# Optimization experiments

Hardware: AMD Instinct MI355X
Metric: run time of the kernel (lower is better)

The kernel has to match this reference:

```python
import jax, jax.numpy as jnp
import numpy as np

D_MODEL = 1024
ED = 2048        # d_inner = expand_factor * d_model
N = 16           # d_state
DT_RANK = 64     # ceil(d_model/16)
K = 4            # d_conv
B_SZ = 4
L = 512


def _causal_depthwise_conv(u, w, b):
    # u: [B, L, ED], w: [ED, 1, K], b: [ED]
    xc = jnp.transpose(u, (0, 2, 1))  # [B, ED, L]
    xc = jax.lax.conv_general_dilated(
        xc, w, window_strides=(1,), padding=[(K - 1, 0)],
        feature_group_count=ED, dimension_numbers=('NCH', 'OIH', 'NCH'))
    xc = xc + b[None, :, None]
    return jnp.transpose(xc, (0, 2, 1))  # [B, L, ED]


def _ssm_branch(xz_half, z, conv_w, conv_b, Wx, Wdt, b_dt, A_log, Dp):
    # xz_half, z: [B, L, ED]
    x = jax.nn.silu(_causal_depthwise_conv(xz_half, conv_w, conv_b))
    dbc = x @ Wx.T  # [B, L, dt_rank + 2N]
    delta = dbc[..., :DT_RANK]
    Bm = dbc[..., DT_RANK:DT_RANK + N]
    Cm = dbc[..., DT_RANK + N:]
    delta = jax.nn.softplus(delta @ Wdt.T + b_dt)  # [B, L, ED]
    A = -jnp.exp(A_log)  # [ED, N]
    dA = jnp.exp(delta[..., None] * A)                        # [B, L, ED, N]
    bx = (delta[..., None] * Bm[:, :, None, :]) * x[..., None]  # [B, L, ED, N]
    dA_t = jnp.transpose(dA, (1, 0, 2, 3))
    bx_t = jnp.transpose(bx, (1, 0, 2, 3))
    c_t = jnp.transpose(Cm, (1, 0, 2))  # [L, B, N]
    h0 = jnp.zeros((x.shape[0], ED, N), dtype=x.dtype)

    def step(h, inp):
        dAi, bxi, ci = inp
        h = dAi * h + bxi
        return h, jnp.einsum('ben,bn->be', h, ci)

    _, ys = jax.lax.scan(step, h0, (dA_t, bx_t, c_t))
    y = jnp.transpose(ys, (1, 0, 2)) + Dp * x  # D skip connection
    return y * jax.nn.silu(z)                  # gate


def _mamba_block(x, W_in, conv_w, conv_b, Wx, Wdt, b_dt, A_log, Dp,
                 conv_w_b, conv_b_b, Wx_b, Wdt_b, b_dt_b, A_log_b, Dp_b, W_out):
    xz = x @ W_in.T  # [B, L, 2*ED]
    xf, zf = xz[..., :ED], xz[..., ED:]
    y = _ssm_branch(xf, zf, conv_w, conv_b, Wx, Wdt, b_dt, A_log, Dp)
    xz_r = xz[:, ::-1, :]
    xb, zb = xz_r[..., :ED], xz_r[..., ED:]
    y_b = _ssm_branch(xb, zb, conv_w_b, conv_b_b, Wx_b, Wdt_b, b_dt_b, A_log_b, Dp_b)
    y = (y + y_b[:, ::-1, :]) * 0.5
    return y @ W_out.T


def setup_inputs() -> dict:
    key = jax.random.key(0)
    ks = jax.random.split(key, 20)
    s = lambda k, shp, sc: jax.random.normal(k, shp, dtype=jnp.float32) * sc
    dt = jnp.exp(jax.random.uniform(ks[15], (ED,)) * (np.log(0.1) - np.log(0.001)) + np.log(0.001))
    dt = jnp.clip(dt, 1e-4, None)
    inv_dt = dt + jnp.log(-jnp.expm1(-dt))
    A_init = jnp.log(jnp.tile(jnp.arange(1, N + 1, dtype=jnp.float32), (ED, 1)))
    return {
        'x': s(ks[0], (B_SZ, L, D_MODEL), 1.0),
        'W_in': s(ks[1], (2 * ED, D_MODEL), D_MODEL ** -0.5),
        'conv_w': s(ks[2], (ED, 1, K), K ** -0.5),
        'conv_b': s(ks[3], (ED,), 0.02),
        'Wx': s(ks[4], (DT_RANK + 2 * N, ED), ED ** -0.5),
        'Wdt': jax.random.uniform(ks[5], (ED, DT_RANK), minval=-DT_RANK ** -0.5, maxval=DT_RANK ** -0.5),
        'b_dt': inv_dt,
        'A_log': A_init,
        'Dp': jnp.ones((ED,), dtype=jnp.float32),
        'conv_w_b': s(ks[6], (ED, 1, K), K ** -0.5),
        'conv_b_b': s(ks[7], (ED,), 0.02),
        'Wx_b': s(ks[8], (DT_RANK + 2 * N, ED), ED ** -0.5),
        'Wdt_b': jax.random.uniform(ks[9], (ED, DT_RANK), minval=-DT_RANK ** -0.5, maxval=DT_RANK ** -0.5),
        'b_dt_b': inv_dt,
        'A_log_b': A_init,
        'Dp_b': jnp.ones((ED,), dtype=jnp.float32),
        'W_out': s(ks[10], (D_MODEL, ED), ED ** -0.5),
    }


def reference(x, W_in, conv_w, conv_b, Wx, Wdt, b_dt, A_log, Dp,
              conv_w_b, conv_b_b, Wx_b, Wdt_b, b_dt_b, A_log_b, Dp_b, W_out):
    return _mamba_block(x, W_in, conv_w, conv_b, Wx, Wdt, b_dt, A_log, Dp,
                        conv_w_b, conv_b_b, Wx_b, Wdt_b, b_dt_b, A_log_b, Dp_b, W_out)
```

## Files before the change

### kernel.cpp

```cpp
#include <hip/hip_runtime.h>
#include <hip/hip_bf16.h>
#include <stdint.h>

typedef unsigned short ushort_t;
typedef __attribute__((ext_vector_type(8))) short short8;
typedef __attribute__((ext_vector_type(4))) float f32x4;

__device__ __forceinline__ float b2f(ushort_t u) {
    union { uint32_t i; float f; } v; v.i = ((uint32_t)u) << 16; return v.f;
}
__device__ __forceinline__ ushort_t f2b(float f) {
    union { float f; uint32_t i; } v; v.f = f;
    uint32_t r = v.i + 0x7fff + ((v.i >> 16) & 1);
    return (ushort_t)(r >> 16);
}

#if __has_builtin(__builtin_amdgcn_exp2f)
#define EXP2(x) __builtin_amdgcn_exp2f(x)
#else
#define EXP2(x) __expf((x) * 0.69314718056f)
#endif

__device__ __forceinline__ void ll16(const ushort_t* g, ushort_t* l) {
    __builtin_amdgcn_global_load_lds(
        (const __attribute__((address_space(1))) uint32_t*)g,
        (__attribute__((address_space(3))) uint32_t*)l, 16, 0, 0);
}

template <int CTRL>
__device__ __forceinline__ float dpp_add(float p) {
    int v = __builtin_amdgcn_update_dpp(0, __float_as_int(p), CTRL, 0xF, 0xF, true);
    return p + __int_as_float(v);
}
#define DPP_XOR1 0xB1
#define DPP_XOR2 0x4E
#define DPP_HMIR 0x141

__device__ __forceinline__ void epi_wave_f32(
    float* sw, const f32x4* accg, float* dst0, int ldc, int lane)
{
    const int quad = lane >> 4, lr = lane & 15;
#pragma unroll
    for (int j = 0; j < 4; j++)
#pragma unroll
        for (int r = 0; r < 4; r++)
            sw[(quad * 4 + r) * 64 + j * 16 + lr] = accg[j][r];
    __asm__ volatile("s_waitcnt lgkmcnt(0)" ::: "memory");
#pragma unroll
    for (int t = 0; t < 4; t++) {
        int row = t * 4 + quad;
        float4 v = *(const float4*)(&sw[row * 64 + lr * 4]);
        *(float4*)(dst0 + (size_t)row * ldc + lr * 4) = v;
    }
}

__device__ __forceinline__ void epi_wave_b16(
    float* sw, const f32x4* accg, ushort_t* dst0, int ldc, int lane)
{
    const int quad = lane >> 4, lr = lane & 15;
#pragma unroll
    for (int j = 0; j < 4; j++)
#pragma unroll
        for (int r = 0; r < 4; r++)
            sw[(quad * 4 + r) * 64 + j * 16 + lr] = accg[j][r];
    __asm__ volatile("s_waitcnt lgkmcnt(0)" ::: "memory");
#pragma unroll
    for (int t = 0; t < 4; t++) {
        int row = t * 4 + quad;
        float4 v = *(const float4*)(&sw[row * 64 + lr * 4]);
        ushort4 o; o.x = f2b(v.x); o.y = f2b(v.y); o.z = f2b(v.z); o.w = f2b(v.w);
        *(ushort4*)(dst0 + (size_t)row * ldc + lr * 4) = o;
    }
}

struct CastSeg { const float4* src; ushort4* dst; };
struct CastArgs { CastSeg seg[7]; int start[8]; };

__global__ __launch_bounds__(256) void cast_multi(CastArgs a)
{
    int g = blockIdx.x * 256 + threadIdx.x;
    if (g >= a.start[7]) return;
    int s = 0;
#pragma unroll
    for (int i = 1; i < 7; i++) s += (g >= a.start[i]);
    int i = g - a.start[s];
    float4 v = a.seg[s].src[i];
    ushort4 o;
    o.x = f2b(v.x); o.y = f2b(v.y); o.z = f2b(v.z); o.w = f2b(v.w);
    a.seg[s].dst[i] = o;
}

#define BK 32

__global__ __launch_bounds__(256) void gemm_g1(
    const ushort_t* __restrict__ A, int lda,
    const ushort_t* __restrict__ B, int ldb,
    ushort_t* __restrict__ Cout, int ldc, int Kd)
{
    __shared__ ushort_t As[128 * BK];
    __shared__ ushort_t Bs[128 * BK];
    __shared__ float sepi[4][1024];

    const int tid  = threadIdx.x;
    const int m0   = blockIdx.y * 128;
    const int n0   = blockIdx.x * 128;
    const int wv   = tid >> 6;
    const int lane = tid & 63;
    const int wm   = (wv >> 1) * 64;
    const int wn   = (wv & 1) * 64;
    const int lr   = lane & 15;
    const int quad = lane >> 4;

    f32x4 acc[4][4];
#pragma unroll
    for (int i = 0; i < 4; i++)
#pragma unroll
        for (int j = 0; j < 4; j++) acc[i][j] = f32x4{0.f, 0.f, 0.f, 0.f};

    const int srA = wv * 32 + (lane >> 2);
    const int scA = (lane & 3) * 8;

    for (int k0 = 0; k0 < Kd; k0 += BK) {
        ll16(A + (size_t)(m0 + srA) * lda + k0 + scA,      &As[wv * 1024]);
        ll16(A + (size_t)(m0 + srA + 16) * lda + k0 + scA, &As[wv * 1024 + 512]);
        ll16(B + (size_t)(n0 + srA) * ldb + k0 + scA,      &Bs[wv * 1024]);
        ll16(B + (size_t)(n0 + srA + 16) * ldb + k0 + scA, &Bs[wv * 1024 + 512]);
        __syncthreads();

        short8 af[4], bf[4];
#pragma unroll
        for (int i = 0; i < 4; i++)
            af[i] = *(const short8*)(&As[(wm + i * 16 + lr) * BK + quad * 8]);
#pragma unroll
        for (int j = 0; j < 4; j++)
            bf[j] = *(const short8*)(&Bs[(wn + j * 16 + lr) * BK + quad * 8]);
#pragma unroll
        for (int i = 0; i < 4; i++)
#pragma unroll
            for (int j = 0; j < 4; j++)
                acc[i][j] = __builtin_amdgcn_mfma_f32_16x16x32_bf16(af[i], bf[j], acc[i][j], 0, 0, 0);
        __syncthreads();
    }

#pragma unroll
    for (int g = 0; g < 4; g++)
        epi_wave_b16(sepi[wv], acc[g],
                     Cout + (size_t)(m0 + wm + g * 16) * ldc + n0 + wn, ldc, lane);
}

__global__ __launch_bounds__(256) void gemm_g4(
    const ushort_t* __restrict__ A, int lda,
    const ushort_t* __restrict__ B, int ldb,
    float* __restrict__ Cout, int ldc, int Kd)
{
    __shared__ ushort_t As[64 * BK];
    __shared__ ushort_t Bs[128 * BK];
    __shared__ float sepi[4][1024];

    const int tid  = threadIdx.x;
    const int m0   = blockIdx.y * 64;
    const int n0   = blockIdx.x * 128;
    const int wv   = tid >> 6;
    const int lane = tid & 63;
    const int wm   = (wv >> 1) * 32;
    const int wn   = (wv & 1) * 64;
    const int lr   = lane & 15;
    const int quad = lane >> 4;

    f32x4 acc[2][4];
#pragma unroll
    for (int i = 0; i < 2; i++)
#pragma unroll
        for (int j = 0; j < 4; j++) acc[i][j] = f32x4{0.f, 0.f, 0.f, 0.f};

    const int srA = wv * 16 + (lane >> 2);
    const int srB = wv * 32 + (lane >> 2);
    const int sc  = (lane & 3) * 8;

    for (int k0 = 0; k0 < Kd; k0 += BK) {
        ll16(A + (size_t)(m0 + srA) * lda + k0 + sc,      &As[wv * 512]);
        ll16(B + (size_t)(n0 + srB) * ldb + k0 + sc,      &Bs[wv * 1024]);
        ll16(B + (size_t)(n0 + srB + 16) * ldb + k0 + sc, &Bs[wv * 1024 + 512]);
        __syncthreads();

        short8 af[2], bf[4];
#pragma unroll
        for (int i = 0; i < 2; i++)
            af[i] = *(const short8*)(&As[(wm + i * 16 + lr) * BK + quad * 8]);
#pragma unroll
        for (int j = 0; j < 4; j++)
            bf[j] = *(const short8*)(&Bs[(wn + j * 16 + lr) * BK + quad * 8]);
#pragma unroll
        for (int i = 0; i < 2; i++)
#pragma unroll
            for (int j = 0; j < 4; j++)
                acc[i][j] = __builtin_amdgcn_mfma_f32_16x16x32_bf16(af[i], bf[j], acc[i][j], 0, 0, 0);
        __syncthreads();
    }

#pragma unroll
    for (int g = 0; g < 2; g++)
        epi_wave_f32(sepi[wv], acc[g],
                     Cout + (size_t)(m0 + wm + g * 16) * ldc + n0 + wn, ldc, lane);
}

__global__ __launch_bounds__(256) void gemm_g2(
    const ushort_t* __restrict__ xc, const ushort_t* __restrict__ wx,
    float* __restrict__ part)
{
    __shared__ ushort_t As[128 * BK];
    __shared__ ushort_t Bs[128 * BK];
    __shared__ float sepi[4][1024];

    const int sk = blockIdx.x, mb = blockIdx.y, br = blockIdx.z;
    const ushort_t* A = xc + (size_t)br * 2048 * 2048;
    const ushort_t* B = wx + (size_t)br * 96 * 2048;
    float* C = part + (size_t)(sk * 2 + br) * 2048 * 96;
    const int m0 = mb * 128;
    const int kb = sk * 256;

    const int tid  = threadIdx.x;
    const int wv   = tid >> 6;
    const int lane = tid & 63;
    const int wm   = (wv >> 1) * 64;
    const int wn   = (wv & 1) * 64;
    const int lr   = lane & 15;
    const int quad = lane >> 4;

    f32x4 acc[4][4];
#pragma unroll
    for (int i = 0; i < 4; i++)
#pragma unroll
        for (int j = 0; j < 4; j++) acc[i][j] = f32x4{0.f, 0.f, 0.f, 0.f};

    const int srA = wv * 32 + (lane >> 2);
    const int sc  = (lane & 3) * 8;

    for (int k0 = kb; k0 < kb + 256; k0 += BK) {
        ll16(A + (size_t)(m0 + srA) * 2048 + k0 + sc,      &As[wv * 1024]);
        ll16(A + (size_t)(m0 + srA + 16) * 2048 + k0 + sc, &As[wv * 1024 + 512]);
        ll16(B + (size_t)(srA) * 2048 + k0 + sc,           &Bs[wv * 1024]);
        ll16(B + (size_t)(srA + 16) * 2048 + k0 + sc,      &Bs[wv * 1024 + 512]);
        __syncthreads();

        short8 af[4], bf[4];
#pragma unroll
        for (int i = 0; i < 4; i++)
            af[i] = *(const short8*)(&As[(wm + i * 16 + lr) * BK + quad * 8]);
#pragma unroll
        for (int j = 0; j < 4; j++)
            bf[j] = *(const short8*)(&Bs[(wn + j * 16 + lr) * BK + quad * 8]);
#pragma unroll
        for (int i = 0; i < 4; i++)
#pragma unroll
            for (int j = 0; j < 4; j++)
                acc[i][j] = __builtin_amdgcn_mfma_f32_16x16x32_bf16(af[i], bf[j], acc[i][j], 0, 0, 0);
        __syncthreads();
    }

    float* sw = sepi[wv];
#pragma unroll
    for (int g = 0; g < 4; g++) {
#pragma unroll
        for (int j = 0; j < 4; j++)
#pragma unroll
            for (int r = 0; r < 4; r++)
                sw[(quad * 4 + r) * 64 + j * 16 + lr] = acc[g][j][r];
        __asm__ volatile("s_waitcnt lgkmcnt(0)" ::: "memory");
        int col = wn + lr * 4;
#pragma unroll
        for (int t = 0; t < 4; t++) {
            int row = t * 4 + quad;
            if (col < 96) {
                float4 v = *(const float4*)(&sw[row * 64 + lr * 4]);
                *(float4*)(C + (size_t)(m0 + wm + g * 16 + row) * 96 + col) = v;
            }
        }
    }
}

__global__ __launch_bounds__(256) void reduce_dbc(
    const float4* __restrict__ part, ushort4* __restrict__ dbc16)
{
    int g = blockIdx.x * 256 + threadIdx.x;
    const int S = 2 * 2048 * 96 / 4;
    float4 r = part[g];
#pragma unroll
    for (int i = 1; i < 8; i++) {
        float4 p = part[g + i * S];
        r.x += p.x; r.y += p.y; r.z += p.z; r.w += p.w;
    }
    ushort4 o; o.x = f2b(r.x); o.y = f2b(r.y); o.z = f2b(r.z); o.w = f2b(r.w);
    dbc16[g] = o;
}

__global__ __launch_bounds__(256) void gemm_g3(
    const ushort_t* __restrict__ dbc16, const ushort_t* __restrict__ wdt,
    ushort_t* __restrict__ delta,
    const float* __restrict__ bdt_f, const float* __restrict__ bdt_b)
{
    __shared__ ushort_t As[128 * BK];
    __shared__ ushort_t Bs[128 * BK];
    __shared__ float sepi[4][1024];

    const int br = blockIdx.z;
    const ushort_t* A = dbc16 + (size_t)br * 2048 * 96;
    const ushort_t* B = wdt + (size_t)br * 2048 * 64;
    ushort_t* C = delta + (size_t)br * 2048 * 2048;
    const float* bias = br ? bdt_b : bdt_f;

    const int tid  = threadIdx.x;
    const int m0   = blockIdx.y * 128;
    const int n0   = blockIdx.x * 128;
    const int wv   = tid >> 6;
    const int lane = tid & 63;
    const int wm   = (wv >> 1) * 64;
    const int wn   = (wv & 1) * 64;
    const int lr   = lane & 15;
    const int quad = lane >> 4;

    f32x4 acc[4][4];
#pragma unroll
    for (int i = 0; i < 4; i++)
#pragma unroll
        for (int j = 0; j < 4; j++) acc[i][j] = f32x4{0.f, 0.f, 0.f, 0.f};

    const int srA = wv * 32 + (lane >> 2);
    const int sc  = (lane & 3) * 8;

    for (int k0 = 0; k0 < 64; k0 += BK) {
        ll16(A + (size_t)(m0 + srA) * 96 + k0 + sc,       &As[wv * 1024]);
        ll16(A + (size_t)(m0 + srA + 16) * 96 + k0 + sc,  &As[wv * 1024 + 512]);
        ll16(B + (size_t)(n0 + srA) * 64 + k0 + sc,       &Bs[wv * 1024]);
        ll16(B + (size_t)(n0 + srA + 16) * 64 + k0 + sc,  &Bs[wv * 1024 + 512]);
        __syncthreads();

        short8 af[4], bf[4];
#pragma unroll
        for (int i = 0; i < 4; i++)
            af[i] = *(const short8*)(&As[(wm + i * 16 + lr) * BK + quad * 8]);
#pragma unroll
        for (int j = 0; j < 4; j++)
            bf[j] = *(const short8*)(&Bs[(wn + j * 16 + lr) * BK + quad * 8]);
#pragma unroll
        for (int i = 0; i < 4; i++)
#pragma unroll
            for (int j = 0; j < 4; j++)
                acc[i][j] = __builtin_amdgcn_mfma_f32_16x16x32_bf16(af[i], bf[j], acc[i][j], 0, 0, 0);
        __syncthreads();
    }

    float bn[4];
#pragma unroll
    for (int j = 0; j < 4; j++) bn[j] = bias[n0 + wn + j * 16 + lr];
#pragma unroll
    for (int g = 0; g < 4; g++)
#pragma unroll
        for (int j = 0; j < 4; j++)
#pragma unroll
            for (int r = 0; r < 4; r++) {
                float x = acc[g][j][r] + bn[j];
                float sp = fmaxf(x, 0.f) + __logf(1.f + __expf(-fabsf(x)));
                acc[g][j][r] = sp;
            }

#pragma unroll
    for (int g = 0; g < 4; g++)
        epi_wave_b16(sepi[wv], acc[g],
                     C + (size_t)(m0 + wm + g * 16) * 2048 + n0 + wn, 2048, lane);
}

__global__ __launch_bounds__(256) void conv_silu_kernel(
    const ushort_t* __restrict__ xz,
    const float* __restrict__ w_f, const float* __restrict__ cb_f,
    const float* __restrict__ w_b, const float* __restrict__ cb_b,
    ushort_t* __restrict__ xc16)
{
    int g = blockIdx.x * 256 + threadIdx.x;
    int e  = g & 2047;
    int t  = (g >> 11) & 511;
    int b  = (g >> 20) & 3;
    int br = g >> 22;

    const float* w  = br ? w_b  : w_f;
    const float* cb = br ? cb_b : cb_f;

    float acc = cb[e];
    float4 wv = *(const float4*)(w + e * 4);
    float wk[4] = { wv.x, wv.y, wv.z, wv.w };

#pragma unroll
    for (int k = 0; k < 4; k++) {
        int tp = t - 3 + k;
        if (tp >= 0) {
            int row = br ? (511 - tp) : tp;
            acc += wk[k] * b2f(xz[((size_t)(b * 512 + row)) * 4096 + e]);
        }
    }
    float s = acc / (1.f + __expf(-acc));
    xc16[g] = f2b(s);
}

__global__ __launch_bounds__(256) void scan_kernel(
    const ushort_t* __restrict__ delta,
    const ushort_t* __restrict__ xc,
    const ushort_t* __restrict__ dbc16,
    const ushort_t* __restrict__ xz,
    const float* __restrict__ Alog_f, const float* __restrict__ Alog_b,
    const float* __restrict__ Dp_f,   const float* __restrict__ Dp_b,
    ushort_t* __restrict__ yf, ushort_t* __restrict__ yb)
{
    const int blk = blockIdx.x;
    const int eg = blk & 63;
    const int b  = (blk >> 6) & 3;
    const int br = blk >> 8;
    const int e0 = eg * 32;

    const int tid = threadIdx.x;
    const int n2  = tid & 7;
    const int el  = tid >> 3;
    const int e   = e0 + el;

    const float* Alog = br ? Alog_b : Alog_f;
    const float* Dpp  = br ? Dp_b   : Dp_f;
    const float A0 = -__expf(Alog[e * 16 + n2]) * 1.44269504f;
    const float A1 = -__expf(Alog[e * 16 + n2 + 8]) * 1.44269504f;

    size_t tb = ((size_t)br * 4 + b) * 512;
    const ushort_t* dlt  = delta + tb * 2048;
    const ushort_t* xcb  = xc    + tb * 2048;
    const ushort_t* dbcb = dbc16 + tb * 96;
    ushort_t* y = (br ? yb : yf) + (size_t)b * 512 * 2048;

    __shared__ float    sd [2][32][68];
    __shared__ float    sdx[2][32][68];
    __shared__ float    sB [2][16][68];
    __shared__ float    sC [2][16][68];
    __shared__ float    sy [2][64][36];

    const int stt = tid >> 2;
    const int seg = tid & 3;
    const int swz = seg * 8;
    const int scol = stt ^ swz;

    float4 rD0 = *(const float4*)(Dpp + e0 + seg * 8);
    float4 rD1 = *(const float4*)(Dpp + e0 + seg * 8 + 4);

    uint4 rdx, rx, rbc, rz;
    uint4 rx_c, rx_f, rz_c, rz_f;

    auto load_regs = [&](int c) {
        int t0 = c * 64;
        rdx = *(const uint4*)(dlt + (size_t)(t0 + stt) * 2048 + e0 + seg * 8);
        rx  = *(const uint4*)(xcb + (size_t)(t0 + stt) * 2048 + e0 + seg * 8);
        rbc = *(const uint4*)(dbcb + (size_t)(t0 + stt) * 96 + 64 + seg * 8);
        int orow = br ? (511 - (t0 + stt)) : (t0 + stt);
        rz  = *(const uint4*)(xz + ((size_t)(b * 512 + orow)) * 4096 + 2048 + e0 + seg * 8);
    };
    auto write_lds = [&](int buf) {
        const uint32_t dw[4] = { rdx.x, rdx.y, rdx.z, rdx.w };
        const uint32_t xw[4] = { rx.x, rx.y, rx.z, rx.w };
#pragma unroll
        for (int k = 0; k < 4; k++) {
            float d0 = b2f((ushort_t)(dw[k] & 0xffff));
            float d1 = b2f((ushort_t)(dw[k] >> 16));
            float x0 = b2f((ushort_t)(xw[k] & 0xffff));
            float x1 = b2f((ushort_t)(xw[k] >> 16));
            sd [buf][seg * 8 + 2 * k][scol]     = d0;
            sd [buf][seg * 8 + 2 * k + 1][scol] = d1;
            sdx[buf][seg * 8 + 2 * k][scol]     = d0 * x0;
            sdx[buf][seg * 8 + 2 * k + 1][scol] = d1 * x1;
        }
        float* arr = (seg < 2) ? &sB[buf][0][0] : &sC[buf][0][0];
        const int rbase = (seg & 1) * 8;
        const uint32_t bw[4] = { rbc.x, rbc.y, rbc.z, rbc.w };
#pragma unroll
        for (int k = 0; k < 4; k++) {
            arr[(rbase + 2 * k) * 68 + scol]     = b2f((ushort_t)(bw[k] & 0xffff));
            arr[(rbase + 2 * k + 1) * 68 + scol] = b2f((ushort_t)(bw[k] >> 16));
        }
    };
    auto flush = [&](int cm1) {
        const int bufm1 = cm1 & 1;
        int row = cm1 * 64 + stt;
        const uint32_t zw[4] = { rz_f.x, rz_f.y, rz_f.z, rz_f.w };
        float zv[8];
#pragma unroll
        for (int k = 0; k < 4; k++) {
            zv[2 * k]     = b2f((ushort_t)(zw[k] & 0xffff));
            zv[2 * k + 1] = b2f((ushort_t)(zw[k] >> 16));
        }
        float4 p0 = *(const float4*)(&sy[bufm1][stt][seg * 8]);
        float4 p1 = *(const float4*)(&sy[bufm1][stt][seg * 8 + 4]);
        const float pv[8] = { p0.x, p0.y, p0.z, p0.w, p1.x, p1.y, p1.z, p1.w };
        const uint32_t xw[4] = { rx_f.x, rx_f.y, rx_f.z, rx_f.w };
        float xvv[8];
#pragma unroll
        for (int k = 0; k < 4; k++) {
            xvv[2 * k]     = b2f((ushort_t)(xw[k] & 0xffff));
            xvv[2 * k + 1] = b2f((ushort_t)(xw[k] >> 16));
        }
        const float Dv[8] = { rD0.x, rD0.y, rD0.z, rD0.w, rD1.x, rD1.y, rD1.z, rD1.w };
        uint32_t op[4];
#pragma unroll
        for (int k = 0; k < 4; k++) {
            float ga = (pv[2 * k]     + Dv[2 * k]     * xvv[2 * k])     *
                       (zv[2 * k]     / (1.f + __expf(-zv[2 * k])));
            float gb = (pv[2 * k + 1] + Dv[2 * k + 1] * xvv[2 * k + 1]) *
                       (zv[2 * k + 1] / (1.f + __expf(-zv[2 * k + 1])));
            op[k] = (uint32_t)f2b(ga) | ((uint32_t)f2b(gb) << 16);
        }
        *(uint4*)(y + (size_t)row * 2048 + e0 + seg * 8) =
            make_uint4(op[0], op[1], op[2], op[3]);
    };

    float h0 = 0.f, h1 = 0.f;
    const int sw = ((el >> 3) & 3) * 8;

    load_regs(0);
    write_lds(0);
    rx_c = rx; rz_c = rz;

    for (int c = 0; c < 8; ++c) {
        if (c < 7) load_regs(c + 1);
        __syncthreads();
        const int buf = c & 1;

        auto LDQ = [&](int tq, float4& dv, float4& dxv, float4& B0, float4& B1,
                       float4& C0, float4& C1) {
            const int tc = tq ^ sw;
            dv  = *(const float4*)(&sd [buf][el][tc]);
            dxv = *(const float4*)(&sdx[buf][el][tc]);
            B0  = *(const float4*)(&sB[buf][n2][tq]);
            B1  = *(const float4*)(&sB[buf][n2 + 8][tq ^ 8]);
            C0  = *(const float4*)(&sC[buf][n2][tq ^ 16]);
            C1  = *(const float4*)(&sC[buf][n2 + 8][tq ^ 24]);
        };

        float4 dv_p, dxv_p, B0_p, B1_p, C0_p, C1_p;
        LDQ(0, dv_p, dxv_p, B0_p, B1_p, C0_p, C1_p);

#pragma unroll 4
        for (int tq = 0; tq < 64; tq += 4) {
            const float4 dv = dv_p, dxv = dxv_p;
            const float4 B0 = B0_p, B1 = B1_p, C0 = C0_p, C1 = C1_p;
            LDQ((tq + 4) & 63, dv_p, dxv_p, B0_p, B1_p, C0_p, C1_p);

            float e00 = EXP2(dv.x * A0), e01 = EXP2(dv.y * A0);
            float e02 = EXP2(dv.z * A0), e03 = EXP2(dv.w * A0);
            float e10 = EXP2(dv.x * A1), e11 = EXP2(dv.y * A1);
            float e12 = EXP2(dv.z * A1), e13 = EXP2(dv.w * A1);

            h0 = e00 * h0 + dxv.x * B0.x;  h1 = e10 * h1 + dxv.x * B1.x;
            float p0 = h0 * C0.x + h1 * C1.x;
            h0 = e01 * h0 + dxv.y * B0.y;  h1 = e11 * h1 + dxv.y * B1.y;
            float p1 = h0 * C0.y + h1 * C1.y;
            h0 = e02 * h0 + dxv.z * B0.z;  h1 = e12 * h1 + dxv.z * B1.z;
            float p2 = h0 * C0.z + h1 * C1.z;
            h0 = e03 * h0 + dxv.w * B0.w;  h1 = e13 * h1 + dxv.w * B1.w;
            float p3 = h0 * C0.w + h1 * C1.w;

            p0 = dpp_add<DPP_XOR1>(p0); p0 = dpp_add<DPP_XOR2>(p0); p0 = dpp_add<DPP_HMIR>(p0);
            p1 = dpp_add<DPP_XOR1>(p1); p1 = dpp_add<DPP_XOR2>(p1); p1 = dpp_add<DPP_HMIR>(p1);
            p2 = dpp_add<DPP_XOR1>(p2); p2 = dpp_add<DPP_XOR2>(p2); p2 = dpp_add<DPP_HMIR>(p2);
            p3 = dpp_add<DPP_XOR1>(p3); p3 = dpp_add<DPP_XOR2>(p3); p3 = dpp_add<DPP_HMIR>(p3);

            if (n2 == 0) {
                sy[buf][tq + 0][el] = p0;
                sy[buf][tq + 1][el] = p1;
                sy[buf][tq + 2][el] = p2;
                sy[buf][tq + 3][el] = p3;
            }
        }

        if (c > 0) flush(c - 1);

        if (c < 7) {
            write_lds((c + 1) & 1);
            rx_f = rx_c; rz_f = rz_c;
            rx_c = rx;   rz_c = rz;
        } else {
            rx_f = rx_c; rz_f = rz_c;
        }
    }
    __syncthreads();
    flush(7);
}

__global__ __launch_bounds__(256) void combine_kernel(
    const uint2* __restrict__ yf, const uint2* __restrict__ yb,
    uint2* __restrict__ yc)
{
    int g = blockIdx.x * 256 + threadIdx.x;
    int e4 = g & 511;
    int t  = (g >> 9) & 511;
    int b  = g >> 18;
    uint2 a = yf[g];
    uint2 c = yb[((size_t)(b * 512 + 511 - t)) * 512 + e4];
    uint2 o;
    o.x = (uint32_t)f2b(0.5f * (b2f((ushort_t)(a.x & 0xffff)) + b2f((ushort_t)(c.x & 0xffff)))) |
          ((uint32_t)f2b(0.5f * (b2f((ushort_t)(a.x >> 16)) + b2f((ushort_t)(c.x >> 16)))) << 16);
    o.y = (uint32_t)f2b(0.5f * (b2f((ushort_t)(a.y & 0xffff)) + b2f((ushort_t)(c.y & 0xffff)))) |
          ((uint32_t)f2b(0.5f * (b2f((ushort_t)(a.y >> 16)) + b2f((ushort_t)(c.y >> 16)))) << 16);
    yc[g] = o;
}

static const size_t TT = 2048;
static const size_t OFF_XZ16  = 0;
static const size_t OFF_XC16  = OFF_XZ16  + TT*4096*2;
static const size_t OFF_DBC16 = OFF_XC16  + 2*TT*2048*2;
static const size_t OFF_DELTA = OFF_DBC16 + 2*TT*96*2;
static const size_t OFF_YF    = OFF_DELTA + 2*TT*2048*2;
static const size_t OFF_YB    = OFF_YF    + TT*2048*2;
static const size_t OFF_YC16  = OFF_YB    + TT*2048*2;
static const size_t OFF_X16   = OFF_YC16  + TT*2048*2;
static const size_t OFF_WIN16 = OFF_X16   + TT*1024*2;
static const size_t OFF_WX16  = OFF_WIN16 + 4096*1024*2;
static const size_t OFF_WDT16 = OFF_WX16  + 2*96*2048*2;
static const size_t OFF_WOUT16= OFF_WDT16 + 2*2048*64*2;
static const size_t OFF_PART  = OFF_WOUT16+ 1024*2048*2;

extern "C" void kernel_launch(void* const* d_in, const int* in_sizes, int n_in,
                              void* d_out, int out_size, void* d_ws, size_t ws_size,
                              hipStream_t stream) {
    const float* x       = (const float*)d_in[0];
    const float* W_in    = (const float*)d_in[1];
    const float* conv_w  = (const float*)d_in[2];
    const float* conv_b  = (const float*)d_in[3];
    const float* Wx      = (const float*)d_in[4];
    const float* Wdt     = (const float*)d_in[5];
    const float* b_dt    = (const float*)d_in[6];
    const float* A_log   = (const float*)d_in[7];
    const float* Dp      = (const float*)d_in[8];
    const float* conv_w_b= (const float*)d_in[9];
    const float* conv_b_b= (const float*)d_in[10];
    const float* Wx_b    = (const float*)d_in[11];
    const float* Wdt_b   = (const float*)d_in[12];
    const float* b_dt_b  = (const float*)d_in[13];
    const float* A_log_b = (const float*)d_in[14];
    const float* Dp_b    = (const float*)d_in[15];
    const float* W_out   = (const float*)d_in[16];
    float* out = (float*)d_out;

    char* ws = (char*)d_ws;
    ushort_t* xz16  = (ushort_t*)(ws + OFF_XZ16);
    ushort_t* xc16  = (ushort_t*)(ws + OFF_XC16);
    ushort_t* dbc16 = (ushort_t*)(ws + OFF_DBC16);
    ushort_t* delta = (ushort_t*)(ws + OFF_DELTA);
    ushort_t* yf    = (ushort_t*)(ws + OFF_YF);
    ushort_t* yb    = (ushort_t*)(ws + OFF_YB);
    ushort_t* yc16  = (ushort_t*)(ws + OFF_YC16);
    ushort_t* x16   = (ushort_t*)(ws + OFF_X16);
    ushort_t* win16 = (ushort_t*)(ws + OFF_WIN16);
    ushort_t* wx16  = (ushort_t*)(ws + OFF_WX16);
    ushort_t* wdt16 = (ushort_t*)(ws + OFF_WDT16);
    ushort_t* wout16= (ushort_t*)(ws + OFF_WOUT16);
    float*    part  = (float*)(ws + OFF_PART);

    dim3 blk(256);

    CastArgs ca;
    const int n4s[7] = {524288, 1048576, 49152, 49152, 32768, 32768, 524288};
    ca.seg[0] = { (const float4*)x,     (ushort4*)x16 };
    ca.seg[1] = { (const float4*)W_in,  (ushort4*)win16 };
    ca.seg[2] = { (const float4*)Wx,    (ushort4*)wx16 };
    ca.seg[3] = { (const float4*)Wx_b,  (ushort4*)(wx16 + 96 * 2048) };
    ca.seg[4] = { (const float4*)Wdt,   (ushort4*)wdt16 };
    ca.seg[5] = { (const float4*)Wdt_b, (ushort4*)(wdt16 + 2048 * 64) };
    ca.seg[6] = { (const float4*)W_out, (ushort4*)wout16 };
    ca.start[0] = 0;
    for (int i = 0; i < 7; i++) ca.start[i + 1] = ca.start[i] + n4s[i];
    cast_multi<<<(ca.start[7] + 255) / 256, blk, 0, stream>>>(ca);

    gemm_g1<<<dim3(32, 16), blk, 0, stream>>>(x16, 1024, win16, 1024, xz16, 4096, 1024);

    conv_silu_kernel<<<32768, blk, 0, stream>>>(xz16, conv_w, conv_b, conv_w_b, conv_b_b, xc16);

    gemm_g2<<<dim3(8, 16, 2), blk, 0, stream>>>(xc16, wx16, part);
    reduce_dbc<<<384, blk, 0, stream>>>((const float4*)part, (ushort4*)dbc16);

    gemm_g3<<<dim3(16, 16, 2), blk, 0, stream>>>(dbc16, wdt16, delta, b_dt, b_dt_b);

    scan_kernel<<<512, blk, 0, stream>>>(delta, xc16, dbc16, xz16, A_log, A_log_b, Dp, Dp_b, yf, yb);

    combine_kernel<<<4096, blk, 0, stream>>>((const uint2*)yf, (const uint2*)yb, (uint2*)yc16);

    gemm_g4<<<dim3(8, 32), blk, 0, stream>>>(yc16, 2048, wout16, 2048, out, 1024, 2048);
}
```

Measured before the change: 276.4 us.

## Shrink scan chunk to 32 steps, pack state as float2, raise occupancy

The selective-scan kernel now processes 32-timestep chunks instead of 64, which halves the shared-memory tiles, and requests 4 blocks per SM through launch bounds. B and C are stored interleaved in pairs so the two state halves can be updated with packed float2 arithmetic, and the swizzles are replaced by padding. The aim is higher occupancy and fewer instructions per step, which hides latency better. The cost is twice as many chunk iterations and barriers, narrower global loads, and possible register spills under the tighter bound.

Result: no change. 274.0 us (-0.9%).

```diff
diff --git a/kernel.cpp b/kernel.cpp
--- a/kernel.cpp
+++ b/kernel.cpp
@@ -5,6 +5,7 @@
 typedef unsigned short ushort_t;
 typedef __attribute__((ext_vector_type(8))) short short8;
 typedef __attribute__((ext_vector_type(4))) float f32x4;
+typedef __attribute__((ext_vector_type(2))) float f32x2;
 
 __device__ __forceinline__ float b2f(ushort_t u) {
     union { uint32_t i; float f; } v; v.i = ((uint32_t)u) << 16; return v.f;
@@ -401,7 +402,7 @@
     xc16[g] = f2b(s);
 }
 
-__global__ __launch_bounds__(256) void scan_kernel(
+__global__ __launch_bounds__(256, 4) void scan_kernel(
     const ushort_t* __restrict__ delta,
     const ushort_t* __restrict__ xc,
     const ushort_t* __restrict__ dbc16,
@@ -423,8 +424,9 @@
 
     const float* Alog = br ? Alog_b : Alog_f;
     const float* Dpp  = br ? Dp_b   : Dp_f;
-    const float A0 = -__expf(Alog[e * 16 + n2]) * 1.44269504f;
-    const float A1 = -__expf(Alog[e * 16 + n2 + 8]) * 1.44269504f;
+    f32x2 a01;
+    a01.x = -__expf(Alog[e * 16 + n2]) * 1.44269504f;
+    a01.y = -__expf(Alog[e * 16 + n2 + 8]) * 1.44269504f;
 
     size_t tb = ((size_t)br * 4 + b) * 512;
     const ushort_t* dlt  = delta + tb * 2048;
@@ -432,150 +434,146 @@
     const ushort_t* dbcb = dbc16 + tb * 96;
     ushort_t* y = (br ? yb : yf) + (size_t)b * 512 * 2048;
 
-    __shared__ float    sd [2][32][68];
-    __shared__ float    sdx[2][32][68];
-    __shared__ float    sB [2][16][68];
-    __shared__ float    sC [2][16][68];
-    __shared__ float    sy [2][64][36];
-
-    const int stt = tid >> 2;
-    const int seg = tid & 3;
-    const int swz = seg * 8;
-    const int scol = stt ^ swz;
-
-    float4 rD0 = *(const float4*)(Dpp + e0 + seg * 8);
-    float4 rD1 = *(const float4*)(Dpp + e0 + seg * 8 + 4);
-
-    uint4 rdx, rx, rbc, rz;
-    uint4 rx_c, rx_f, rz_c, rz_f;
+    __shared__ float sd [2][32][36];
+    __shared__ float sdx[2][32][36];
+    __shared__ float sBp[2][8][34][2];
+    __shared__ float sCp[2][8][34][2];
+    __shared__ float sy [2][32][33];
+
+    const int stt = tid >> 3;
+    const int seg = tid & 7;
+    const int sg4 = seg * 4;
+
+    float4 rD = *(const float4*)(Dpp + e0 + sg4);
+
+    uint2 rdx, rx, rbc, rz;
+    uint2 rx_c, rx_f, rz_c, rz_f;
 
     auto load_regs = [&](int c) {
-        int t0 = c * 64;
-        rdx = *(const uint4*)(dlt + (size_t)(t0 + stt) * 2048 + e0 + seg * 8);
-        rx  = *(const uint4*)(xcb + (size_t)(t0 + stt) * 2048 + e0 + seg * 8);
-        rbc = *(const uint4*)(dbcb + (size_t)(t0 + stt) * 96 + 64 + seg * 8);
-        int orow = br ? (511 - (t0 + stt)) : (t0 + stt);
-        rz  = *(const uint4*)(xz + ((size_t)(b * 512 + orow)) * 4096 + 2048 + e0 + seg * 8);
+        int row = c * 32 + stt;
+        rdx = *(const uint2*)(dlt + (size_t)row * 2048 + e0 + sg4);
+        rx  = *(const uint2*)(xcb + (size_t)row * 2048 + e0 + sg4);
+        rbc = *(const uint2*)(dbcb + (size_t)row * 96 + 64 + sg4);
+        int orow = br ? (511 - row) : row;
+        rz  = *(const uint2*)(xz + ((size_t)(b * 512 + orow)) * 4096 + 2048 + e0 + sg4);
     };
     auto write_lds = [&](int buf) {
-        const uint32_t dw[4] = { rdx.x, rdx.y, rdx.z, rdx.w };
-        const uint32_t xw[4] = { rx.x, rx.y, rx.z, rx.w };
-#pragma unroll
-        for (int k = 0; k < 4; k++) {
+        const uint32_t dw[2] = { rdx.x, rdx.y };
+        const uint32_t xw[2] = { rx.x, rx.y };
+#pragma unroll
+        for (int k = 0; k < 2; k++) {
             float d0 = b2f((ushort_t)(dw[k] & 0xffff));
             float d1 = b2f((ushort_t)(dw[k] >> 16));
             float x0 = b2f((ushort_t)(xw[k] & 0xffff));
             float x1 = b2f((ushort_t)(xw[k] >> 16));
-            sd [buf][seg * 8 + 2 * k][scol]     = d0;
-            sd [buf][seg * 8 + 2 * k + 1][scol] = d1;
-            sdx[buf][seg * 8 + 2 * k][scol]     = d0 * x0;
-            sdx[buf][seg * 8 + 2 * k + 1][scol] = d1 * x1;
-        }
-        float* arr = (seg < 2) ? &sB[buf][0][0] : &sC[buf][0][0];
-        const int rbase = (seg & 1) * 8;
-        const uint32_t bw[4] = { rbc.x, rbc.y, rbc.z, rbc.w };
-#pragma unroll
-        for (int k = 0; k < 4; k++) {
-            arr[(rbase + 2 * k) * 68 + scol]     = b2f((ushort_t)(bw[k] & 0xffff));
-            arr[(rbase + 2 * k + 1) * 68 + scol] = b2f((ushort_t)(bw[k] >> 16));
+            sd [buf][sg4 + 2 * k][stt]     = d0;
+            sd [buf][sg4 + 2 * k + 1][stt] = d1;
+            sdx[buf][sg4 + 2 * k][stt]     = d0 * x0;
+            sdx[buf][sg4 + 2 * k + 1][stt] = d1 * x1;
+        }
+        float* arr = (seg < 4) ? &sBp[buf][0][0][0] : &sCp[buf][0][0][0];
+        const int nb = (seg & 3) * 4;
+        const uint32_t bw[2] = { rbc.x, rbc.y };
+#pragma unroll
+        for (int k = 0; k < 2; k++) {
+            int na = nb + 2 * k, nbd = nb + 2 * k + 1;
+            arr[(na  & 7) * 68 + stt * 2 + (na  >> 3)] = b2f((ushort_t)(bw[k] & 0xffff));
+            arr[(nbd & 7) * 68 + stt * 2 + (nbd >> 3)] = b2f((ushort_t)(bw[k] >> 16));
         }
     };
     auto flush = [&](int cm1) {
         const int bufm1 = cm1 & 1;
-        int row = cm1 * 64 + stt;
-        const uint32_t zw[4] = { rz_f.x, rz_f.y, rz_f.z, rz_f.w };
-        float zv[8];
-#pragma unroll
-        for (int k = 0; k < 4; k++) {
+        int row = cm1 * 32 + stt;
+        const uint32_t zw[2] = { rz_f.x, rz_f.y };
+        float zv[4];
+#pragma unroll
+        for (int k = 0; k < 2; k++) {
             zv[2 * k]     = b2f((ushort_t)(zw[k] & 0xffff));
             zv[2 * k + 1] = b2f((ushort_t)(zw[k] >> 16));
         }
-        float4 p0 = *(const float4*)(&sy[bufm1][stt][seg * 8]);
-        float4 p1 = *(const float4*)(&sy[bufm1][stt][seg * 8 + 4]);
-        const float pv[8] = { p0.x, p0.y, p0.z, p0.w, p1.x, p1.y, p1.z, p1.w };
-        const uint32_t xw[4] = { rx_f.x, rx_f.y, rx_f.z, rx_f.w };
-        float xvv[8];
-#pragma unroll
-        for (int k = 0; k < 4; k++) {
+        float pv[4];
+#pragma unroll
+        for (int k = 0; k < 4; k++) pv[k] = sy[bufm1][stt][sg4 + k];
+        const uint32_t xw[2] = { rx_f.x, rx_f.y };
+        float xvv[4];
+#pragma unroll
+        for (int k = 0; k < 2; k++) {
             xvv[2 * k]     = b2f((ushort_t)(xw[k] & 0xffff));
             xvv[2 * k + 1] = b2f((ushort_t)(xw[k] >> 16));
         }
-        const float Dv[8] = { rD0.x, rD0.y, rD0.z, rD0.w, rD1.x, rD1.y, rD1.z, rD1.w };
-        uint32_t op[4];
-#pragma unroll
-        for (int k = 0; k < 4; k++) {
+        const float Dv[4] = { rD.x, rD.y, rD.z, rD.w };
+        uint32_t op[2];
+#pragma unroll
+        for (int k = 0; k < 2; k++) {
             float ga = (pv[2 * k]     + Dv[2 * k]     * xvv[2 * k])     *
                        (zv[2 * k]     / (1.f + __expf(-zv[2 * k])));
             float gb = (pv[2 * k + 1] + Dv[2 * k + 1] * xvv[2 * k + 1]) *
                        (zv[2 * k + 1] / (1.f + __expf(-zv[2 * k + 1])));
             op[k] = (uint32_t)f2b(ga) | ((uint32_t)f2b(gb) << 16);
         }
-        *(uint4*)(y + (size_t)row * 2048 + e0 + seg * 8) =
-            make_uint4(op[0], op[1], op[2], op[3]);
+        *(uint2*)(y + (size_t)row * 2048 + e0 + sg4) = make_uint2(op[0], op[1]);
     };
 
-    float h0 = 0.f, h1 = 0.f;
-    const int sw = ((el >> 3) & 3) * 8;
+    f32x2 h01 = f32x2{0.f, 0.f};
 
     load_regs(0);
     write_lds(0);
     rx_c = rx; rz_c = rz;
 
-    for (int c = 0; c < 8; ++c) {
-        if (c < 7) load_regs(c + 1);
+    for (int c = 0; c < 16; ++c) {
+        if (c < 15) load_regs(c + 1);
         __syncthreads();
         const int buf = c & 1;
 
-        auto LDQ = [&](int tq, float4& dv, float4& dxv, float4& B0, float4& B1,
-                       float4& C0, float4& C1) {
-            const int tc = tq ^ sw;
-            dv  = *(const float4*)(&sd [buf][el][tc]);
-            dxv = *(const float4*)(&sdx[buf][el][tc]);
-            B0  = *(const float4*)(&sB[buf][n2][tq]);
-            B1  = *(const float4*)(&sB[buf][n2 + 8][tq ^ 8]);
-            C0  = *(const float4*)(&sC[buf][n2][tq ^ 16]);
-            C1  = *(const float4*)(&sC[buf][n2 + 8][tq ^ 24]);
+        auto LDQ = [&](int tq, f32x4& dv, f32x4& dxv, f32x4& bq0, f32x4& bq1,
+                       f32x4& cq0, f32x4& cq1) {
+            dv  = *(const f32x4*)(&sd [buf][el][tq]);
+            dxv = *(const f32x4*)(&sdx[buf][el][tq]);
+            bq0 = *(const f32x4*)(&sBp[buf][n2][tq][0]);
+            bq1 = *(const f32x4*)(&sBp[buf][n2][tq + 2][0]);
+            cq0 = *(const f32x4*)(&sCp[buf][n2][tq][0]);
+            cq1 = *(const f32x4*)(&sCp[buf][n2][tq + 2][0]);
         };
 
-        float4 dv_p, dxv_p, B0_p, B1_p, C0_p, C1_p;
-        LDQ(0, dv_p, dxv_p, B0_p, B1_p, C0_p, C1_p);
-
+        f32x4 dv_p, dxv_p, bq0_p, bq1_p, cq0_p, cq1_p;
+        LDQ(0, dv_p, dxv_p, bq0_p, bq1_p, cq0_p, cq1_p);
+
+        float pout[4];
 #pragma unroll 4
-        for (int tq = 0; tq < 64; tq += 4) {
-            const float4 dv = dv_p, dxv = dxv_p;
-            const float4 B0 = B0_p, B1 = B1_p, C0 = C0_p, C1 = C1_p;
-            LDQ((tq + 4) & 63, dv_p, dxv_p, B0_p, B1_p, C0_p, C1_p);
-
-            float e00 = EXP2(dv.x * A0), e01 = EXP2(dv.y * A0);
-            float e02 = EXP2(dv.z * A0), e03 = EXP2(dv.w * A0);
-            float e10 = EXP2(dv.x * A1), e11 = EXP2(dv.y * A1);
-            float e12 = EXP2(dv.z * A1), e13 = EXP2(dv.w * A1);
-
-            h0 = e00 * h0 + dxv.x * B0.x;  h1 = e10 * h1 + dxv.x * B1.x;
-            float p0 = h0 * C0.x + h1 * C1.x;
-            h0 = e01 * h0 + dxv.y * B0.y;  h1 = e11 * h1 + dxv.y * B1.y;
-            float p1 = h0 * C0.y + h1 * C1.y;
-            h0 = e02 * h0 + dxv.z * B0.z;  h1 = e12 * h1 + dxv.z * B1.z;
-            float p2 = h0 * C0.z + h1 * C1.z;
-            h0 = e03 * h0 + dxv.w * B0.w;  h1 = e13 * h1 + dxv.w * B1.w;
-            float p3 = h0 * C0.w + h1 * C1.w;
-
-            p0 = dpp_add<DPP_XOR1>(p0); p0 = dpp_add<DPP_XOR2>(p0); p0 = dpp_add<DPP_HMIR>(p0);
-            p1 = dpp_add<DPP_XOR1>(p1); p1 = dpp_add<DPP_XOR2>(p1); p1 = dpp_add<DPP_HMIR>(p1);
-            p2 = dpp_add<DPP_XOR1>(p2); p2 = dpp_add<DPP_XOR2>(p2); p2 = dpp_add<DPP_HMIR>(p2);
-            p3 = dpp_add<DPP_XOR1>(p3); p3 = dpp_add<DPP_XOR2>(p3); p3 = dpp_add<DPP_HMIR>(p3);
+        for (int tq = 0; tq < 32; tq += 4) {
+            const f32x4 dv = dv_p, dxv = dxv_p;
+            const f32x4 bq0 = bq0_p, bq1 = bq1_p, cq0 = cq0_p, cq1 = cq1_p;
+            LDQ((tq + 4) & 31, dv_p, dxv_p, bq0_p, bq1_p, cq0_p, cq1_p);
+
+#define SSTEP(DC, DXC, BT, CT, TI)                                   \
+            {                                                        \
+                f32x2 arg = a01 * (DC);                              \
+                f32x2 ee; ee.x = EXP2(arg.x); ee.y = EXP2(arg.y);    \
+                h01 = ee * h01 + (BT) * (DXC);                       \
+                f32x2 pp = h01 * (CT);                               \
+                float p = pp.x + pp.y;                               \
+                p = dpp_add<DPP_XOR1>(p);                            \
+                p = dpp_add<DPP_XOR2>(p);                            \
+                p = dpp_add<DPP_HMIR>(p);                            \
+                pout[TI] = p;                                        \
+            }
+            SSTEP(dv.x, dxv.x, bq0.xy, cq0.xy, 0)
+            SSTEP(dv.y, dxv.y, bq0.zw, cq0.zw, 1)
+            SSTEP(dv.z, dxv.z, bq1.xy, cq1.xy, 2)
+            SSTEP(dv.w, dxv.w, bq1.zw, cq1.zw, 3)
+#undef SSTEP
 
             if (n2 == 0) {
-                sy[buf][tq + 0][el] = p0;
-                sy[buf][tq + 1][el] = p1;
-                sy[buf][tq + 2][el] = p2;
-                sy[buf][tq + 3][el] = p3;
+                sy[buf][tq + 0][el] = pout[0];
+                sy[buf][tq + 1][el] = pout[1];
+                sy[buf][tq + 2][el] = pout[2];
+                sy[buf][tq + 3][el] = pout[3];
             }
         }
 
         if (c > 0) flush(c - 1);
 
-        if (c < 7) {
+        if (c < 15) {
             write_lds((c + 1) & 1);
             rx_f = rx_c; rz_f = rz_c;
             rx_c = rx;   rz_c = rz;
@@ -584,7 +582,7 @@
         }
     }
     __syncthreads();
-    flush(7);
+    flush(15);
 }
 
 __global__ __launch_bounds__(256) void combine_kernel(
```
